# Performance work log

Measured on AMD Instinct MI355X. Metric: run time of the kernel, lower is better.

The kernel has to match this reference:

```python
import jax, jax.numpy as jnp
import numpy as np

TK = 3          # number of temporal scales (wavedec level = TK-1)
SK = 3          # spatial rank count per scale (SK-1 rank-1 terms + residual)
INPUT_LEN = 256
N_NODES = 256
K = 32          # randomized-SVD sketch size
INV_SQRT2 = np.float32(1.0 / np.sqrt(2.0))


def haar_wavedec(x, levels):
    # x: (..., L) with L divisible by 2**levels; pywt haar, mode='zero', even L
    # returns [cD1, cD2, ..., cD_levels, cA_levels]  (== pywt.wavedec(...)[::-1])
    coeffs = []
    for _ in range(levels):
        L = x.shape[-1]
        pairs = x.reshape(x.shape[:-1] + (L // 2, 2))
        a, b = pairs[..., 0], pairs[..., 1]
        coeffs.append((a - b) * INV_SQRT2)  # detail cD
        x = (a + b) * INV_SQRT2             # approx cA
    coeffs.append(x)
    return coeffs


def setup_inputs() -> dict:
    key = jax.random.key(0)
    kx, kp = jax.random.split(key)
    x = jax.random.normal(kx, (4, INPUT_LEN, 64, N_NODES), dtype=jnp.float32)
    p = jax.random.normal(kp, (N_NODES, K), dtype=jnp.float32)
    return {"x": x, "p": p}


def reference(x, p):
    # x: (B, T, c, n) -> permute(0,2,3,1) -> (B, c, n, T)
    xw = jnp.transpose(x, (0, 2, 3, 1))
    coeffs = haar_wavedec(xw, TK - 1)  # TK tensors (B, c, n, L_i)
    res = []
    for xi in coeffs:
        if SK == 1:
            res.append(xi)
            continue
        xt = jnp.transpose(xi, (0, 3, 1, 2))          # (B, L, c, n)
        z = xt @ p                                     # (B, L, c, k)
        q, _ = jnp.linalg.qr(z)                        # reduced: (B, L, c, k)
        y = jnp.einsum('blck,blcn->blkn', q, xt)       # (B, L, k, n)
        u, s, vh = jnp.linalg.svd(y, full_matrices=False)  # u:(B,L,k,k) s:(B,L,k) vh:(B,L,k,n)
        u = q @ u                                      # (B, L, c, k)
        # rank-1 terms s_j * u_j v_j^T for j < SK-1, vectorized over j
        terms = jnp.einsum('blcj,blj,bljn->jblcn',
                           u[..., :SK - 1], s[..., :SK - 1], vh[..., :SK - 1, :])
        terms = jnp.transpose(terms, (0, 1, 3, 4, 2))  # (SK-1, B, c, n, L)
        resid = xi - terms.sum(axis=0)
        for j in range(SK - 1):
            res.append(terms[j])
        res.append(resid)
    # left-pad last dim to INPUT_LEN, then stack -> (TK*SK, B, c, n, INPUT_LEN)
    res = [jnp.pad(r, ((0, 0), (0, 0), (0, 0), (INPUT_LEN - r.shape[-1], 0))) for r in res]
    return jnp.stack(res)
```

## Files before the change

### kernel.cpp

```cpp
#include <hip/hip_runtime.h>

#define IS2f 0.70710678118654752440f

#define WS_Z   0ul
#define WS_G   2097152ul
#define WS_H   3145728ul
#define WS_SU  4194304ul
#define WS_VV  4325376ul
#define WS_B   4849664ul

#define WSYNC() asm volatile("" ::: "memory")

__device__ __forceinline__ float frcp(float v){ return __builtin_amdgcn_rcpf(v); }
__device__ __forceinline__ float frsq(float v){ return __builtin_amdgcn_rsqf(v); }
__device__ __forceinline__ float fsq (float v){ return __builtin_amdgcn_sqrtf(v); }
__device__ __forceinline__ float readlane_f(float v, int sl){
  return __uint_as_float(__builtin_amdgcn_readlane(__float_as_uint(v), sl));
}

__device__ __forceinline__ void decode_pid(int pid, int& ci, int& b, int& l, int& L){
  if (pid < 512)      { ci = 0; b = pid >> 7; l = pid & 127; L = 128; }
  else if (pid < 768) { int q = pid - 512; ci = 1; b = q >> 6; l = q & 63; L = 64; }
  else                { int q = pid - 768; ci = 2; b = q >> 6; l = q & 63; L = 64; }
}
__device__ __forceinline__ int su_base(int ci){ return ci==0 ? 0 : (ci==1 ? 65536 : 98304); }
__device__ __forceinline__ int vv_base(int ci){ return ci==0 ? 0 : (ci==1 ? 262144 : 393216); }
__device__ __forceinline__ int tpp(int r, int m){ return (m==0) ? r  : (r+m)%31; }
__device__ __forceinline__ int tqq(int r, int m){ return (m==0) ? 31 : (r+31-m)%31; }

#define PTS 260

__global__ __launch_bounds__(256) void k_fact(const float* __restrict__ x,
                                              const float* __restrict__ p,
                                              float* __restrict__ ws, int storeB){
  __shared__ __align__(16) float Ms[64*256];
  __shared__ __align__(16) float Zs[64*32];
  __shared__ __align__(16) float Pt[32*PTS];
  __shared__ __align__(16) float Bn[32*PTS];

  int pid = blockIdx.x, tid = threadIdx.x;
  int ci,b,l,L; decode_pid(pid,ci,b,l,L);

  {
    const float4* p4 = (const float4*)p;
    #pragma unroll
    for (int e=0;e<8;++e){
      int idx = tid + 256*e;
      int n = idx >> 3, k4 = idx & 7;
      float4 v = p4[idx];
      Pt[(4*k4+0)*PTS + n] = v.x;
      Pt[(4*k4+1)*PTS + n] = v.y;
      Pt[(4*k4+2)*PTS + n] = v.z;
      Pt[(4*k4+3)*PTS + n] = v.w;
    }
  }
  const float4* x4 = (const float4*)x;
  float4* Ms4 = (float4*)Ms;
  if (ci == 0){
    size_t base = ((size_t)(b*256 + 2*l) * 64) * 64;
    #pragma unroll
    for (int e=0;e<16;++e){
      int f = tid + 256*e;
      float4 A = x4[base + f];
      float4 Bv = x4[base + 4096 + f];
      float4 m;
      m.x=(A.x-Bv.x)*IS2f; m.y=(A.y-Bv.y)*IS2f; m.z=(A.z-Bv.z)*IS2f; m.w=(A.w-Bv.w)*IS2f;
      Ms4[f] = m;
    }
  } else {
    float sg = (ci==1) ? -0.5f : 0.5f;
    size_t base = ((size_t)(b*256 + 4*l) * 64) * 64;
    #pragma unroll
    for (int e=0;e<16;++e){
      int f = tid + 256*e;
      float4 A = x4[base + f];
      float4 B1 = x4[base + 4096 + f];
      float4 C1 = x4[base + 8192 + f];
      float4 D1 = x4[base + 12288 + f];
      float4 m;
      m.x=(A.x+B1.x)*0.5f + (C1.x+D1.x)*sg;
      m.y=(A.y+B1.y)*0.5f + (C1.y+D1.y)*sg;
      m.z=(A.z+B1.z)*0.5f + (C1.z+D1.z)*sg;
      m.w=(A.w+B1.w)*0.5f + (C1.w+D1.w)*sg;
      Ms4[f] = m;
    }
  }
  __syncthreads();

  {
    int k = tid & 31, c0 = tid >> 5;
    float acc[8] = {0,0,0,0,0,0,0,0};
    for (int n4=0;n4<64;++n4){
      float4 pv = *(const float4*)&Pt[k*PTS + 4*n4];
      #pragma unroll
      for (int i=0;i<8;++i){
        float4 m = Ms4[(c0*8+i)*64 + n4];
        acc[i] += m.x*pv.x + m.y*pv.y + m.z*pv.z + m.w*pv.w;
      }
    }
    #pragma unroll
    for (int i=0;i<8;++i){
      int c = c0*8 + i;
      Zs[c*32+k] = acc[i];
      ws[WS_Z + (size_t)pid*2048 + c*32 + k] = acc[i];
    }
  }
  __syncthreads();

  {
    int kk = tid & 31, j0 = tid >> 5;
    float ga[4] = {0,0,0,0};
    for (int c=0;c<64;++c){
      float zk = Zs[c*32+kk];
      #pragma unroll
      for (int e=0;e<4;++e) ga[e] += Zs[c*32 + j0 + 8*e] * zk;
    }
    #pragma unroll
    for (int e=0;e<4;++e)
      ws[WS_G + (size_t)pid*1024 + (j0+8*e)*32 + kk] = ga[e];
  }

  {
    int n4 = tid & 63, kg = tid >> 6;
    float4 facc[8];
    #pragma unroll
    for (int kq=0;kq<8;++kq){ facc[kq].x=0.f; facc[kq].y=0.f; facc[kq].z=0.f; facc[kq].w=0.f; }
    for (int c=0;c<64;++c){
      float4 mv = Ms4[c*64 + n4];
      float4 z1 = *(const float4*)&Zs[c*32 + kg*8];
      float4 z2 = *(const float4*)&Zs[c*32 + kg*8 + 4];
      float zz[8] = {z1.x,z1.y,z1.z,z1.w,z2.x,z2.y,z2.z,z2.w};
      #pragma unroll
      for (int kq=0;kq<8;++kq){
        facc[kq].x += zz[kq]*mv.x; facc[kq].y += zz[kq]*mv.y;
        facc[kq].z += zz[kq]*mv.z; facc[kq].w += zz[kq]*mv.w;
      }
    }
    #pragma unroll
    for (int kq=0;kq<8;++kq){
      int krow = kg*8 + kq;
      *(float4*)&Bn[krow*PTS + 4*n4] = facc[kq];
      if (storeB)
        *(float4*)&ws[WS_B + (size_t)pid*8192 + (size_t)krow*256 + 4*n4] = facc[kq];
    }
  }
  __syncthreads();

  {
    int kk = tid & 31, j0 = tid >> 5;
    float h[4] = {0,0,0,0};
    for (int n4=0;n4<64;++n4){
      float4 bk = *(const float4*)&Bn[kk*PTS + 4*n4];
      #pragma unroll
      for (int e=0;e<4;++e){
        float4 bj = *(const float4*)&Bn[(j0+8*e)*PTS + 4*n4];
        h[e] += bj.x*bk.x + bj.y*bk.y + bj.z*bk.z + bj.w*bk.w;
      }
    }
    #pragma unroll
    for (int e=0;e<4;++e)
      ws[WS_H + (size_t)pid*1024 + (j0+8*e)*32 + kk] = h[e];
  }
}

#define NSWEEP 5

__global__ __launch_bounds__(128) void k_solve(const float* __restrict__ x,
                                               float* __restrict__ ws, int useB){
  __shared__ float Gs[32*33];
  __shared__ float Hs[32*33];
  __shared__ float Vsh[32*33];
  __shared__ float cA[16], sA[16];
  __shared__ float ggs[2][32];
  __shared__ float uss[2][64];

  int pid = blockIdx.x, tid = threadIdx.x;
  int wave = tid >> 6;
  int lane = tid & 63;
  int jlane = tid & 31;
  int wv4  = tid >> 5;
  int hlf  = (tid >> 5) & 1;
  int ci,b,l,L; decode_pid(pid,ci,b,l,L);

  #pragma unroll
  for (int e=0;e<8;++e){
    int idx = tid + 128*e; int i = idx>>5, j = idx&31;
    Gs[i*33+j]  = ws[WS_G + (size_t)pid*1024 + idx];
    Hs[i*33+j]  = ws[WS_H + (size_t)pid*1024 + idx];
    Vsh[i*33+j] = (i==j) ? 1.f : 0.f;
  }
  __syncthreads();

  for (int k=0;k<32;++k){
    float gkk  = Gs[k*33+k];
    float ginv = frcp(gkk);
    float gkj  = Gs[k*33+jlane];
    float av[8], bv[8];
    #pragma unroll
    for (int e=0;e<8;++e){
      int i = k+1+wv4+4*e; int ii = (i<32)? i : 31;
      av[e] = Gs[ii*33+jlane];
      bv[e] = Gs[k*33+ii];
    }
    WSYNC();
    #pragma unroll
    for (int e=0;e<8;++e){
      int i = k+1+wv4+4*e;
      if (i < 32) Gs[i*33+jlane] = av[e] - bv[e]*gkj*ginv;
    }
    __syncthreads();
  }
  {
    float sv[8];
    #pragma unroll
    for (int e=0;e<8;++e){
      int i = wv4+4*e;
      float d = Gs[i*33+i];
      sv[e] = Gs[i*33+jlane] * frsq(d);
    }
    WSYNC();
    #pragma unroll
    for (int e=0;e<8;++e){
      int i = wv4+4*e;
      Gs[i*33+jlane] = sv[e];
    }
  }
  __syncthreads();

  for (int i=0;i<32;++i){
    float rinv = frcp(Gs[i*33+i]);
    float hs   = Hs[i*33+jlane] * rinv;
    float av[8], bv[8];
    #pragma unroll
    for (int e=0;e<8;++e){
      int m = i+1+wv4+4*e; int mm = (m<32)? m : 31;
      av[e] = Hs[mm*33+jlane];
      bv[e] = Gs[i*33+mm];
    }
    WSYNC();
    #pragma unroll
    for (int e=0;e<8;++e){
      int m = i+1+wv4+4*e;
      if (m < 32) Hs[m*33+jlane] = av[e] - bv[e]*hs;
    }
    __syncthreads();
  }
  {
    float sv[8];
    #pragma unroll
    for (int e=0;e<8;++e){
      int m = wv4+4*e;
      sv[e] = Hs[m*33+jlane] * frcp(Gs[m*33+m]);
    }
    WSYNC();
    #pragma unroll
    for (int e=0;e<8;++e){
      int m = wv4+4*e;
      Hs[m*33+jlane] = sv[e];
    }
  }
  __syncthreads();

  for (int j=0;j<32;++j){
    float rinv = frcp(Gs[j*33+j]);
    float hs   = Hs[jlane*33+j] * rinv;
    float av[8], bv[8];
    #pragma unroll
    for (int e=0;e<8;++e){
      int m = j+1+wv4+4*e; int mm = (m<32)? m : 31;
      av[e] = Hs[jlane*33+mm];
      bv[e] = Gs[j*33+mm];
    }
    WSYNC();
    #pragma unroll
    for (int e=0;e<8;++e){
      int m = j+1+wv4+4*e;
      if (m < 32) Hs[jlane*33+m] = av[e] - bv[e]*hs;
    }
    __syncthreads();
  }
  {
    float sv[8];
    #pragma unroll
    for (int e=0;e<8;++e){
      int m = wv4+4*e;
      sv[e] = Hs[jlane*33+m] * frcp(Gs[m*33+m]);
    }
    WSYNC();
    #pragma unroll
    for (int e=0;e<8;++e){
      int m = wv4+4*e;
      Hs[jlane*33+m] = sv[e];
    }
  }
  __syncthreads();

  float dmx = (lane < 32) ? fabsf(Hs[jlane*33+jlane]) : 0.f;
  #pragma unroll
  for (int off=1; off<64; off<<=1) dmx = fmaxf(dmx, __shfl_xor(dmx, off));
  float thr = dmx * 3e-6f;

  for (int sw=0; sw<NSWEEP; ++sw){
    for (int r=0; r<31; ++r){
      if (wave == 0){
        int m = lane & 15;
        int pm = tpp(r,m), qm = tqq(r,m);
        float app = Hs[pm*33+pm];
        float aqq = Hs[qm*33+qm];
        float apq = Hs[pm*33+qm];
        if (!__ballot(fabsf(apq) > thr)) continue;
        float tau = (aqq - app) * frcp(2.f*apq);
        float tt  = ((tau>=0.f)?1.f:-1.f) * frcp(fabsf(tau) + fsq(fmaf(tau,tau,1.f)));
        float cc  = frsq(fmaf(tt,tt,1.f));
        float ss  = tt*cc;
        bool ok = fabsf(apq) > 1e-28f;
        if (lane < 16){ cA[lane] = ok?cc:1.f; sA[lane] = ok?ss:0.f; }
        WSYNC();

        int m2 = lane >> 2, lm = lane & 3;
        int p2 = tpp(r,m2), q2 = tqq(r,m2);
        float c2 = cA[m2], s2 = sA[m2];
        float a_[4], b_[4], c_[4], d_[4], c1v[4], s1v[4];
        int p1v[4], q1v[4];
        #pragma unroll
        for (int e=0;e<4;++e){
          int m1 = lm + 4*e;
          int p1 = tpp(r,m1), q1 = tqq(r,m1);
          p1v[e]=p1; q1v[e]=q1;
          c1v[e]=cA[m1]; s1v[e]=sA[m1];
          a_[e] = Hs[p1*33+p2]; b_[e] = Hs[p1*33+q2];
          c_[e] = Hs[q1*33+p2]; d_[e] = Hs[q1*33+q2];
        }
        WSYNC();
        #pragma unroll
        for (int e=0;e<4;++e){
          float c1 = c1v[e], s1 = s1v[e];
          float a1 = c1*a_[e] - s1*c_[e];
          float b1 = c1*b_[e] - s1*d_[e];
          float c1r= s1*a_[e] + c1*c_[e];
          float d1 = s1*b_[e] + c1*d_[e];
          Hs[p1v[e]*33+p2] = c2*a1 - s2*b1;
          Hs[p1v[e]*33+q2] = s2*a1 + c2*b1;
          Hs[q1v[e]*33+p2] = c2*c1r - s2*d1;
          Hs[q1v[e]*33+q2] = s2*c1r + c2*d1;
        }
      } else {
        int m2 = lane >> 2, lm = lane & 3;
        int p2 = tpp(r,m2), q2 = tqq(r,m2);
        float app = Hs[p2*33+p2];
        float aqq = Hs[q2*33+q2];
        float apq = Hs[p2*33+q2];
        if (!__ballot(fabsf(apq) > thr)) continue;
        float tau = (aqq - app) * frcp(2.f*apq);
        float tt  = ((tau>=0.f)?1.f:-1.f) * frcp(fabsf(tau) + fsq(fmaf(tau,tau,1.f)));
        float cc  = frsq(fmaf(tt,tt,1.f));
        float ss  = tt*cc;
        bool ok = fabsf(apq) > 1e-28f;
        float c2 = ok?cc:1.f, s2 = ok?ss:0.f;

        float vp[8], vq[8];
        #pragma unroll
        for (int e=0;e<8;++e){
          int i = lm + 4*e;
          vp[e] = Vsh[i*33+p2];
          vq[e] = Vsh[i*33+q2];
        }
        WSYNC();
        #pragma unroll
        for (int e=0;e<8;++e){
          int i = lm + 4*e;
          Vsh[i*33+p2] = c2*vp[e] - s2*vq[e];
          Vsh[i*33+q2] = s2*vp[e] + c2*vq[e];
        }
      }
      __syncthreads();
    }
  }
  __syncthreads();
  if (wave == 1) return;

  float rdgr = frcp(Gs[jlane*33+jlane]);

  float dv = (lane < 32) ? Hs[jlane*33+jlane] : -3e38f;
  float m1r = dv;
  #pragma unroll
  for (int off=1; off<64; off<<=1) m1r = fmaxf(m1r, __shfl_xor(m1r, off));
  unsigned long long bm = __ballot(dv == m1r);
  int i0 = __ffsll((unsigned long long)bm) - 1;
  float dv2 = (lane == i0) ? -3e38f : dv;
  float m2r = dv2;
  #pragma unroll
  for (int off=1; off<64; off<<=1) m2r = fmaxf(m2r, __shfl_xor(m2r, off));
  unsigned long long bm2 = __ballot(dv2 == m2r);
  int i1 = __ffsll((unsigned long long)bm2) - 1;

  float lam = hlf ? m2r : m1r;
  int   ti  = hlf ? i1 : i0;
  float sj  = fsq(fmaxf(lam, 0.f)); sj = fmaxf(sj, 1e-12f);
  float s0 = readlane_f(sj, 0);
  float s1 = readlane_f(sj, 32);

  {
    float rr = Vsh[jlane*33 + ti];
    float Greg[32];
    #pragma unroll
    for (int i=0;i<32;++i) Greg[i] = Gs[jlane*33+i];
    #pragma unroll
    for (int i=31;i>=0;--i){
      float ri = __shfl(rr,  hlf*32 + i);
      float di = __shfl(rdgr, i);
      float g  = ri * di;
      if (jlane == i) ggs[hlf][i] = g;
      if (jlane < i)  rr -= Greg[i]*g;
    }
  }
  WSYNC();

  {
    const float4* Z4 = (const float4*)(ws + WS_Z + (size_t)pid*2048);
    float u0 = 0.f, u1 = 0.f;
    #pragma unroll
    for (int k4=0;k4<8;++k4){
      float4 z = Z4[lane*8 + k4];
      u0 += z.x*ggs[0][k4*4+0] + z.y*ggs[0][k4*4+1] + z.z*ggs[0][k4*4+2] + z.w*ggs[0][k4*4+3];
      u1 += z.x*ggs[1][k4*4+0] + z.y*ggs[1][k4*4+1] + z.z*ggs[1][k4*4+2] + z.w*ggs[1][k4*4+3];
    }
    uss[0][lane] = u0; uss[1][lane] = u1;
    ws[WS_SU + su_base(ci) + ((size_t)(b*2+0)*64 + lane)*L + l] = s0*u0;
    ws[WS_SU + su_base(ci) + ((size_t)(b*2+1)*64 + lane)*L + l] = s1*u1;
  }
  WSYNC();

  float i0s = frcp(s0), i1s = frcp(s1);
  size_t vb0 = WS_VV + vv_base(ci) + ((size_t)(b*2+0)*L + l)*256 + lane*4;
  size_t vb1 = WS_VV + vv_base(ci) + ((size_t)(b*2+1)*L + l)*256 + lane*4;

  if (useB){
    const float4* B4 = (const float4*)(ws + WS_B + (size_t)pid*8192);
    float a0x=0,a0y=0,a0z=0,a0w=0, a1x=0,a1y=0,a1z=0,a1w=0;
    #pragma unroll 8
    for (int k=0;k<32;++k){
      float4 bv = B4[(size_t)k*64 + lane];
      float g0 = ggs[0][k], g1 = ggs[1][k];
      a0x += g0*bv.x; a0y += g0*bv.y; a0z += g0*bv.z; a0w += g0*bv.w;
      a1x += g1*bv.x; a1y += g1*bv.y; a1z += g1*bv.z; a1w += g1*bv.w;
    }
    float4 r0; r0.x=a0x*i0s; r0.y=a0y*i0s; r0.z=a0z*i0s; r0.w=a0w*i0s;
    float4 r1; r1.x=a1x*i1s; r1.y=a1y*i1s; r1.z=a1z*i1s; r1.w=a1w*i1s;
    *(float4*)(ws + vb0) = r0;
    *(float4*)(ws + vb1) = r1;
  } else {
    float a0x=0,a0y=0,a0z=0,a0w=0, a1x=0,a1y=0,a1z=0,a1w=0;
    const float4* x4 = (const float4*)x;
    if (ci == 0){
      size_t base = ((size_t)(b*256 + 2*l) * 64) * 64;
      #pragma unroll 2
      for (int c=0;c<64;++c){
        float4 A  = x4[base + c*64 + lane];
        float4 Bv = x4[base + 4096 + c*64 + lane];
        float mx=(A.x-Bv.x)*IS2f, my=(A.y-Bv.y)*IS2f, mz=(A.z-Bv.z)*IS2f, mw=(A.w-Bv.w)*IS2f;
        float uc0 = uss[0][c], uc1 = uss[1][c];
        a0x += uc0*mx; a0y += uc0*my; a0z += uc0*mz; a0w += uc0*mw;
        a1x += uc1*mx; a1y += uc1*my; a1z += uc1*mz; a1w += uc1*mw;
      }
    } else {
      float sg = (ci==1) ? -0.5f : 0.5f;
      size_t base = ((size_t)(b*256 + 4*l) * 64) * 64;
      #pragma unroll 2
      for (int c=0;c<64;++c){
        float4 A  = x4[base + c*64 + lane];
        float4 B1 = x4[base + 4096 + c*64 + lane];
        float4 C1 = x4[base + 8192 + c*64 + lane];
        float4 D1 = x4[base + 12288 + c*64 + lane];
        float mx=(A.x+B1.x)*0.5f + (C1.x+D1.x)*sg;
        float my=(A.y+B1.y)*0.5f + (C1.y+D1.y)*sg;
        float mz=(A.z+B1.z)*0.5f + (C1.z+D1.z)*sg;
        float mw=(A.w+B1.w)*0.5f + (C1.w+D1.w)*sg;
        float uc0 = uss[0][c], uc1 = uss[1][c];
        a0x += uc0*mx; a0y += uc0*my; a0z += uc0*mz; a0w += uc0*mw;
        a1x += uc1*mx; a1y += uc1*my; a1z += uc1*mz; a1w += uc1*mw;
      }
    }
    ws[vb0+0]=a0x*i0s; ws[vb0+1]=a0y*i0s; ws[vb0+2]=a0z*i0s; ws[vb0+3]=a0w*i0s;
    ws[vb1+0]=a1x*i1s; ws[vb1+1]=a1y*i1s; ws[vb1+2]=a1z*i1s; ws[vb1+3]=a1w*i1s;
  }
}

__global__ __launch_bounds__(256) void k_out(const float* __restrict__ x,
                                             const float* __restrict__ ws,
                                             float* __restrict__ out){
  __shared__ float d1[128*33];
  __shared__ float d2[64*33];
  __shared__ float a2s[64*33];
  __shared__ float Vs[2*128*33];
  __shared__ float Us[512];

  int nt = blockIdx.x, c = blockIdx.y, b = blockIdx.z;
  int n0 = nt * 32, tid = threadIdx.x;
  float* a1 = Vs;

  const float4* x4 = (const float4*)x;
  #pragma unroll
  for (int e=0;e<4;++e){
    int f = tid + 256*e; int l1 = f>>3, d4 = f&7;
    size_t r = ((size_t)(b*256 + 2*l1)*64 + c)*64 + (n0>>2) + d4;
    float4 A = x4[r], Bv = x4[r + 4096];
    int o = l1*33 + 4*d4;
    d1[o+0]=(A.x-Bv.x)*IS2f; d1[o+1]=(A.y-Bv.y)*IS2f; d1[o+2]=(A.z-Bv.z)*IS2f; d1[o+3]=(A.w-Bv.w)*IS2f;
    a1[o+0]=(A.x+Bv.x)*IS2f; a1[o+1]=(A.y+Bv.y)*IS2f; a1[o+2]=(A.z+Bv.z)*IS2f; a1[o+3]=(A.w+Bv.w)*IS2f;
  }
  __syncthreads();
  #pragma unroll
  for (int e=0;e<2;++e){
    int f = tid + 256*e; int l2 = f>>3, d4 = f&7;
    #pragma unroll
    for (int j=0;j<4;++j){
      int dn = 4*d4 + j;
      float aa = a1[(2*l2)*33 + dn], bb = a1[(2*l2+1)*33 + dn];
      d2[l2*33+dn]  = (aa-bb)*IS2f;
      a2s[l2*33+dn] = (aa+bb)*IS2f;
    }
  }
  #pragma unroll
  for (int e=0;e<2;++e){
    int idx = tid + 256*e;
    int j, l, L, so;
    if (idx < 256)      { j=idx>>7;        l=idx&127; L=128; so=0; }
    else if (idx < 384) { j=(idx-256)>>6;  l=idx&63;  L=64;  so=65536; }
    else                { j=(idx-384)>>6;  l=idx&63;  L=64;  so=98304; }
    Us[idx] = ws[WS_SU + so + ((size_t)(b*2+j)*64 + c)*L + l];
  }
  __syncthreads();

  for (int cc=0; cc<3; ++cc){
    int L   = (cc==0) ? 128 : 64;
    int pad = 256 - L;
    int sb  = cc*3;
    int uo  = (cc==0) ? 0 : (cc==1) ? 256 : 384;
    const float* cf = (cc==0) ? d1 : (cc==1) ? d2 : a2s;

    int iters = (2*L*32) >> 8;
    for (int e=0;e<iters;++e){
      int idx = tid + 256*e;
      int j = (idx >= L*32) ? 1 : 0;
      int rem = idx - j*L*32;
      int ll = rem >> 5, dn = rem & 31;
      Vs[j*4224 + ll*33 + dn] =
        ws[WS_VV + vv_base(cc) + ((size_t)(b*2+j)*L + ll)*256 + n0 + dn];
    }
    __syncthreads();

    int l = tid - pad;
    bool inr = (l >= 0);
    size_t obase = (size_t)sb*16777216 + (size_t)b*4194304 + (size_t)c*65536
                 + (size_t)n0*256 + tid;
    #pragma unroll 4
    for (int dn=0; dn<32; ++dn){
      float v0 = 0.f, v1 = 0.f, rv = 0.f;
      if (inr){
        float q0 = Us[uo + l]     * Vs[l*33 + dn];
        float q1 = Us[uo + L + l] * Vs[4224 + l*33 + dn];
        v0 = q0; v1 = q1;
        rv = cf[l*33 + dn] - q0 - q1;
      }
      out[obase + dn*256]            = v0;
      out[obase + dn*256 + 16777216] = v1;
      out[obase + dn*256 + 33554432] = rv;
    }
    __syncthreads();
  }
}

extern "C" void kernel_launch(void* const* d_in, const int* in_sizes, int n_in,
                              void* d_out, int out_size, void* d_ws, size_t ws_size,
                              hipStream_t stream) {
  const float* x = (const float*)d_in[0];
  const float* p = (const float*)d_in[1];
  float* out = (float*)d_out;
  float* ws  = (float*)d_ws;

  int useB = (ws_size >= (size_t)(WS_B + 1024ull*8192ull) * 4ull) ? 1 : 0;

  k_fact <<<1024, 256, 0, stream>>>(x, p, ws, useB);
  k_solve<<<1024, 128, 0, stream>>>(x, ws, useB);
  k_out  <<<dim3(8,64,4), 256, 0, stream>>>(x, ws, out);
}
```

Measured before the change: 466.4 us.

## Double k_solve threads to 256 and spread Jacobi rotations over four waves

```diff
diff --git a/kernel.cpp b/kernel.cpp
--- a/kernel.cpp
+++ b/kernel.cpp
@@ -27,6 +27,16 @@
 __device__ __forceinline__ int vv_base(int ci){ return ci==0 ? 0 : (ci==1 ? 262144 : 393216); }
 __device__ __forceinline__ int tpp(int r, int m){ return (m==0) ? r  : (r+m)%31; }
 __device__ __forceinline__ int tqq(int r, int m){ return (m==0) ? 31 : (r+31-m)%31; }
+__device__ __forceinline__ void jparam(float app, float aqq, float apq,
+                                       float& cc, float& ss){
+  float tau = (aqq - app) * frcp(2.f*apq);
+  float tt  = ((tau>=0.f)?1.f:-1.f) * frcp(fabsf(tau) + fsq(fmaf(tau,tau,1.f)));
+  float c   = frsq(fmaf(tt,tt,1.f));
+  float s   = tt*c;
+  bool ok = fabsf(apq) > 1e-28f;
+  cc = ok ? c : 1.f;
+  ss = ok ? s : 0.f;
+}
 
 #define PTS 260
 
@@ -165,12 +175,11 @@
 
 #define NSWEEP 5
 
-__global__ __launch_bounds__(128) void k_solve(const float* __restrict__ x,
+__global__ __launch_bounds__(256) void k_solve(const float* __restrict__ x,
                                                float* __restrict__ ws, int useB){
   __shared__ float Gs[32*33];
   __shared__ float Hs[32*33];
   __shared__ float Vsh[32*33];
-  __shared__ float cA[16], sA[16];
   __shared__ float ggs[2][32];
   __shared__ float uss[2][64];
 
@@ -178,13 +187,13 @@
   int wave = tid >> 6;
   int lane = tid & 63;
   int jlane = tid & 31;
-  int wv4  = tid >> 5;
+  int wv8  = tid >> 5;
   int hlf  = (tid >> 5) & 1;
   int ci,b,l,L; decode_pid(pid,ci,b,l,L);
 
   #pragma unroll
-  for (int e=0;e<8;++e){
-    int idx = tid + 128*e; int i = idx>>5, j = idx&31;
+  for (int e=0;e<4;++e){
+    int idx = tid + 256*e; int i = idx>>5, j = idx&31;
     Gs[i*33+j]  = ws[WS_G + (size_t)pid*1024 + idx];
     Hs[i*33+j]  = ws[WS_H + (size_t)pid*1024 + idx];
     Vsh[i*33+j] = (i==j) ? 1.f : 0.f;
@@ -195,33 +204,33 @@
     float gkk  = Gs[k*33+k];
     float ginv = frcp(gkk);
     float gkj  = Gs[k*33+jlane];
-    float av[8], bv[8];
-    #pragma unroll
-    for (int e=0;e<8;++e){
-      int i = k+1+wv4+4*e; int ii = (i<32)? i : 31;
+    float av[4], bv[4];
+    #pragma unroll
+    for (int e=0;e<4;++e){
+      int i = k+1+wv8+8*e; int ii = (i<32)? i : 31;
       av[e] = Gs[ii*33+jlane];
       bv[e] = Gs[k*33+ii];
     }
     WSYNC();
     #pragma unroll
-    for (int e=0;e<8;++e){
-      int i = k+1+wv4+4*e;
+    for (int e=0;e<4;++e){
+      int i = k+1+wv8+8*e;
       if (i < 32) Gs[i*33+jlane] = av[e] - bv[e]*gkj*ginv;
     }
     __syncthreads();
   }
   {
-    float sv[8];
-    #pragma unroll
-    for (int e=0;e<8;++e){
-      int i = wv4+4*e;
+    float sv[4];
+    #pragma unroll
+    for (int e=0;e<4;++e){
+      int i = wv8+8*e;
       float d = Gs[i*33+i];
       sv[e] = Gs[i*33+jlane] * frsq(d);
     }
     WSYNC();
     #pragma unroll
-    for (int e=0;e<8;++e){
-      int i = wv4+4*e;
+    for (int e=0;e<4;++e){
+      int i = wv8+8*e;
       Gs[i*33+jlane] = sv[e];
     }
   }
@@ -230,32 +239,32 @@
   for (int i=0;i<32;++i){
     float rinv = frcp(Gs[i*33+i]);
     float hs   = Hs[i*33+jlane] * rinv;
-    float av[8], bv[8];
-    #pragma unroll
-    for (int e=0;e<8;++e){
-      int m = i+1+wv4+4*e; int mm = (m<32)? m : 31;
+    float av[4], bv[4];
+    #pragma unroll
+    for (int e=0;e<4;++e){
+      int m = i+1+wv8+8*e; int mm = (m<32)? m : 31;
       av[e] = Hs[mm*33+jlane];
       bv[e] = Gs[i*33+mm];
     }
     WSYNC();
     #pragma unroll
-    for (int e=0;e<8;++e){
-      int m = i+1+wv4+4*e;
+    for (int e=0;e<4;++e){
+      int m = i+1+wv8+8*e;
       if (m < 32) Hs[m*33+jlane] = av[e] - bv[e]*hs;
     }
     __syncthreads();
   }
   {
-    float sv[8];
-    #pragma unroll
-    for (int e=0;e<8;++e){
-      int m = wv4+4*e;
+    float sv[4];
+    #pragma unroll
+    for (int e=0;e<4;++e){
+      int m = wv8+8*e;
       sv[e] = Hs[m*33+jlane] * frcp(Gs[m*33+m]);
     }
     WSYNC();
     #pragma unroll
-    for (int e=0;e<8;++e){
-      int m = wv4+4*e;
+    for (int e=0;e<4;++e){
+      int m = wv8+8*e;
       Hs[m*33+jlane] = sv[e];
     }
   }
@@ -264,32 +273,32 @@
   for (int j=0;j<32;++j){
     float rinv = frcp(Gs[j*33+j]);
     float hs   = Hs[jlane*33+j] * rinv;
-    float av[8], bv[8];
-    #pragma unroll
-    for (int e=0;e<8;++e){
-      int m = j+1+wv4+4*e; int mm = (m<32)? m : 31;
+    float av[4], bv[4];
+    #pragma unroll
+    for (int e=0;e<4;++e){
+      int m = j+1+wv8+8*e; int mm = (m<32)? m : 31;
       av[e] = Hs[jlane*33+mm];
       bv[e] = Gs[j*33+mm];
     }
     WSYNC();
     #pragma unroll
-    for (int e=0;e<8;++e){
-      int m = j+1+wv4+4*e;
+    for (int e=0;e<4;++e){
+      int m = j+1+wv8+8*e;
       if (m < 32) Hs[jlane*33+m] = av[e] - bv[e]*hs;
     }
     __syncthreads();
   }
   {
-    float sv[8];
-    #pragma unroll
-    for (int e=0;e<8;++e){
-      int m = wv4+4*e;
+    float sv[4];
+    #pragma unroll
+    for (int e=0;e<4;++e){
+      int m = wv8+8*e;
       sv[e] = Hs[jlane*33+m] * frcp(Gs[m*33+m]);
     }
     WSYNC();
     #pragma unroll
-    for (int e=0;e<8;++e){
-      int m = wv4+4*e;
+    for (int e=0;e<4;++e){
+      int m = wv8+8*e;
       Hs[jlane*33+m] = sv[e];
     }
   }
@@ -302,39 +311,33 @@
 
   for (int sw=0; sw<NSWEEP; ++sw){
     for (int r=0; r<31; ++r){
-      if (wave == 0){
+      {
         int m = lane & 15;
-        int pm = tpp(r,m), qm = tqq(r,m);
-        float app = Hs[pm*33+pm];
-        float aqq = Hs[qm*33+qm];
-        float apq = Hs[pm*33+qm];
-        if (!__ballot(fabsf(apq) > thr)) continue;
-        float tau = (aqq - app) * frcp(2.f*apq);
-        float tt  = ((tau>=0.f)?1.f:-1.f) * frcp(fabsf(tau) + fsq(fmaf(tau,tau,1.f)));
-        float cc  = frsq(fmaf(tt,tt,1.f));
-        float ss  = tt*cc;
-        bool ok = fabsf(apq) > 1e-28f;
-        if (lane < 16){ cA[lane] = ok?cc:1.f; sA[lane] = ok?ss:0.f; }
-        WSYNC();
-
-        int m2 = lane >> 2, lm = lane & 3;
+        float apqb = Hs[tpp(r,m)*33 + tqq(r,m)];
+        if (!__ballot(fabsf(apqb) > thr)) continue;
+      }
+      if (wave < 2){
+        int m2 = (lane >> 3) + 8*wave;
+        int lm = lane & 7;
         int p2 = tpp(r,m2), q2 = tqq(r,m2);
-        float c2 = cA[m2], s2 = sA[m2];
-        float a_[4], b_[4], c_[4], d_[4], c1v[4], s1v[4];
-        int p1v[4], q1v[4];
+        float app2 = Hs[p2*33+p2], aqq2 = Hs[q2*33+q2], apq2 = Hs[p2*33+q2];
+        float ap1[2], aq1[2], ax1[2];
+        float a_[2], b_[2], c_[2], d_[2];
+        int p1v[2], q1v[2];
         #pragma unroll
-        for (int e=0;e<4;++e){
-          int m1 = lm + 4*e;
+        for (int e=0;e<2;++e){
+          int m1 = lm + 8*e;
           int p1 = tpp(r,m1), q1 = tqq(r,m1);
           p1v[e]=p1; q1v[e]=q1;
-          c1v[e]=cA[m1]; s1v[e]=sA[m1];
+          ap1[e] = Hs[p1*33+p1]; aq1[e] = Hs[q1*33+q1]; ax1[e] = Hs[p1*33+q1];
           a_[e] = Hs[p1*33+p2]; b_[e] = Hs[p1*33+q2];
           c_[e] = Hs[q1*33+p2]; d_[e] = Hs[q1*33+q2];
         }
-        WSYNC();
+        __syncthreads();
+        float c2, s2; jparam(app2, aqq2, apq2, c2, s2);
         #pragma unroll
-        for (int e=0;e<4;++e){
-          float c1 = c1v[e], s1 = s1v[e];
+        for (int e=0;e<2;++e){
+          float c1, s1; jparam(ap1[e], aq1[e], ax1[e], c1, s1);
           float a1 = c1*a_[e] - s1*c_[e];
           float b1 = c1*b_[e] - s1*d_[e];
           float c1r= s1*a_[e] + c1*c_[e];
@@ -345,30 +348,22 @@
           Hs[q1v[e]*33+q2] = s2*c1r + c2*d1;
         }
       } else {
-        int m2 = lane >> 2, lm = lane & 3;
+        int m2 = (lane >> 3) + 8*(wave-2);
+        int lm = lane & 7;
         int p2 = tpp(r,m2), q2 = tqq(r,m2);
-        float app = Hs[p2*33+p2];
-        float aqq = Hs[q2*33+q2];
-        float apq = Hs[p2*33+q2];
-        if (!__ballot(fabsf(apq) > thr)) continue;
-        float tau = (aqq - app) * frcp(2.f*apq);
-        float tt  = ((tau>=0.f)?1.f:-1.f) * frcp(fabsf(tau) + fsq(fmaf(tau,tau,1.f)));
-        float cc  = frsq(fmaf(tt,tt,1.f));
-        float ss  = tt*cc;
-        bool ok = fabsf(apq) > 1e-28f;
-        float c2 = ok?cc:1.f, s2 = ok?ss:0.f;
-
-        float vp[8], vq[8];
+        float app2 = Hs[p2*33+p2], aqq2 = Hs[q2*33+q2], apq2 = Hs[p2*33+q2];
+        float vp[4], vq[4];
         #pragma unroll
-        for (int e=0;e<8;++e){
-          int i = lm + 4*e;
+        for (int e=0;e<4;++e){
+          int i = lm + 8*e;
           vp[e] = Vsh[i*33+p2];
           vq[e] = Vsh[i*33+q2];
         }
-        WSYNC();
+        __syncthreads();
+        float c2, s2; jparam(app2, aqq2, apq2, c2, s2);
         #pragma unroll
-        for (int e=0;e<8;++e){
-          int i = lm + 4*e;
+        for (int e=0;e<4;++e){
+          int i = lm + 8*e;
           Vsh[i*33+p2] = c2*vp[e] - s2*vq[e];
           Vsh[i*33+q2] = s2*vp[e] + c2*vq[e];
         }
@@ -377,7 +372,7 @@
     }
   }
   __syncthreads();
-  if (wave == 1) return;
+  if (wave != 0) return;
 
   float rdgr = frcp(Gs[jlane*33+jlane]);
 
@@ -582,6 +577,6 @@
   int useB = (ws_size >= (size_t)(WS_B + 1024ull*8192ull) * 4ull) ? 1 : 0;
 
   k_fact <<<1024, 256, 0, stream>>>(x, p, ws, useB);
-  k_solve<<<1024, 128, 0, stream>>>(x, ws, useB);
+  k_solve<<<1024, 256, 0, stream>>>(x, ws, useB);
   k_out  <<<dim3(8,64,4), 256, 0, stream>>>(x, ws, out);
 }
```

Measured after the change: 494.2 us. 1.06x slower.
